# Kernel optimization log

Measured on AMD Instinct MI355X. Metric: run time of the kernel, lower is better.

The kernel has to match this reference:

```python
import jax, jax.numpy as jnp
import numpy as np

NUM_HEADS = 16
EPS = 1e-6  # torch LayerNorm default is 1e-5; module uses nn.LayerNorm default
LN_EPS = 1e-5


def layer_norm(x, w, b, eps=LN_EPS):
    # normalize over last dim (head_dim), matching infer_layer_norm
    mu = jnp.mean(x, axis=-1, keepdims=True)
    xc = x - mu
    var = jnp.mean(xc * xc, axis=-1, keepdims=True)
    return xc / jnp.sqrt(var + eps) * w + b


def setup_inputs() -> dict:
    key = jax.random.key(0)
    ks = jax.random.split(key, 4)
    B, N, C = 2, 4096, 1024
    H = NUM_HEADS
    D = C // H
    x = jax.random.normal(ks[0], (B, N, C), dtype=jnp.float32)
    qkv_w = jax.random.normal(ks[1], (3 * C, C), dtype=jnp.float32) * (C ** -0.5)
    qkv_b = jax.random.normal(ks[2], (3 * C,), dtype=jnp.float32) * 0.02
    q_norm_w = jnp.ones((D,), dtype=jnp.float32)
    q_norm_b = jnp.zeros((D,), dtype=jnp.float32)
    k_norm_w = jnp.ones((D,), dtype=jnp.float32)
    k_norm_b = jnp.zeros((D,), dtype=jnp.float32)
    proj_w = jax.random.normal(ks[3], (C, C), dtype=jnp.float32) * (C ** -0.5)
    proj_b = jnp.zeros((C,), dtype=jnp.float32)
    return {"x": x, "qkv_w": qkv_w, "qkv_b": qkv_b,
            "q_norm_w": q_norm_w, "q_norm_b": q_norm_b,
            "k_norm_w": k_norm_w, "k_norm_b": k_norm_b,
            "proj_w": proj_w, "proj_b": proj_b}


def reference(x, qkv_w, qkv_b, q_norm_w, q_norm_b, k_norm_w, k_norm_b, proj_w, proj_b):
    B, N, C = x.shape
    H = NUM_HEADS
    D = C // H
    scale = D ** -0.5
    # QKV projection: torch Linear uses y = x @ W^T + b
    qkv = x @ qkv_w.T + qkv_b                      # [B,N,3C]
    qkv = qkv.reshape(B, N, 3, H, D).transpose(2, 0, 3, 1, 4)  # [3,B,H,N,D]
    q, k, v = qkv[0], qkv[1], qkv[2]
    # per-head qk layernorm
    q = layer_norm(q, q_norm_w, q_norm_b)
    k = layer_norm(k, k_norm_w, k_norm_b)
    # scaled dot product attention
    attn = jnp.einsum('bhqd,bhkd->bhqk', q * scale, k)
    attn = jax.nn.softmax(attn, axis=-1)
    out = jnp.einsum('bhqk,bhkd->bhqd', attn, v)   # [B,H,N,D]
    out = out.transpose(0, 2, 1, 3).reshape(B, N, C)
    return out @ proj_w.T + proj_b
```

## Files before the change

### kernel.cpp

```cpp
#include <hip/hip_runtime.h>
#include <hip/hip_bf16.h>

#define NB 2
#define NN 4096
#define NC 1024
#define NH 16
#define ND 64
#define NM (NB*NN)
#define NK 1024
#define J_QKV 3072
#define QSCALE 0.18033688011112042f

typedef unsigned short u16;
typedef unsigned int   u32;
typedef __attribute__((ext_vector_type(8)))  __bf16 bf16x8;
typedef __attribute__((ext_vector_type(4)))  float  f32x4;
typedef __attribute__((ext_vector_type(16))) float  f32x16;

__device__ __forceinline__ u16 f2bf(float f) {
    unsigned int i = __builtin_bit_cast(unsigned int, f);
    unsigned int lsb = (i >> 16) & 1u;
    i += 0x7fffu + lsb;
    return (u16)(i >> 16);
}
__device__ __forceinline__ float fast_exp2(float x) {
#if __has_builtin(__builtin_amdgcn_exp2f)
    return __builtin_amdgcn_exp2f(x);
#else
    return exp2f(x);
#endif
}
__device__ __forceinline__ u32 pkbf(float a, float b) {
    u32 r;
    asm("v_cvt_pk_bf16_f32 %0, %1, %2" : "=v"(r) : "v"(a), "v"(b));
    return r;
}
typedef struct { u32 x, y; } u32pair;
__device__ __forceinline__ u32pair swap32(u32 a, u32 b) {
#if __has_builtin(__builtin_amdgcn_permlane32_swap)
    auto r = __builtin_amdgcn_permlane32_swap((int)a, (int)b, false, false);
    u32pair o; o.x = (u32)r[0]; o.y = (u32)r[1]; return o;
#else
    const bool hi = (threadIdx.x & 32) != 0;
    u32 as = (u32)__shfl_xor((int)a, 32);
    u32 bs = (u32)__shfl_xor((int)b, 32);
    u32pair o; o.x = hi ? bs : a; o.y = hi ? b : as; return o;
#endif
}

__device__ __forceinline__ void glds16(const u16* g, u16* l) {
    __builtin_amdgcn_global_load_lds(
        (const __attribute__((address_space(1))) u32*)g,
        (__attribute__((address_space(3))) u32*)l, 16, 0, 0);
}

__global__ __launch_bounds__(256) void cvt_bf16(
    const float* __restrict__ in, u16* __restrict__ out)
{
    const size_t i = ((size_t)blockIdx.x * 256 + threadIdx.x) * 8;
    const float4 a = *(const float4*)(in + i);
    const float4 b = *(const float4*)(in + i + 4);
    union { u16 h[8]; uint4 v; } u;
    u.h[0] = f2bf(a.x); u.h[1] = f2bf(a.y); u.h[2] = f2bf(a.z); u.h[3] = f2bf(a.w);
    u.h[4] = f2bf(b.x); u.h[5] = f2bf(b.y); u.h[6] = f2bf(b.z); u.h[7] = f2bf(b.w);
    *(uint4*)(out + i) = u.v;
}

template<int MODE, int NJB>
__global__ __launch_bounds__(256, 3) void gemm_nt(
    const u16* __restrict__ A, const u16* __restrict__ W,
    const float* __restrict__ bias,
    const float* __restrict__ qw, const float* __restrict__ qb,
    const float* __restrict__ kw, const float* __restrict__ kb,
    void* __restrict__ outv)
{
    __shared__ __align__(16) u16 AsL[128][32];
    __shared__ __align__(16) u16 AsH[128][32];
    __shared__ __align__(16) u16 BsL[128][32];
    __shared__ __align__(16) u16 BsH[128][32];
    const int t = threadIdx.x;
    const int w = t >> 6, lane = t & 63;
    const int nb   = blockIdx.x;
    const int cpx  = gridDim.x >> 3;
    const int nb2  = (nb & 7) * cpx + (nb >> 3);
    const int chunk = nb2 / cpx;
    const int c     = nb2 - chunk * cpx;
    const int jb  = (c >> 3) * 128;
    const int m0  = (chunk * 8 + (c & 7)) * 128;
    const int wr = (w >> 1) * 64, wc = (w & 1) * 64;
    const int srow = t >> 2, skc = (t & 3) * 8;
    const u16* ap0 = A + (size_t)(m0 + srow) * NK + skc;
    const u16* ap1 = ap0 + (size_t)64 * NK;
    const u16* wp0 = W + (size_t)(jb + srow) * NK + skc;
    const u16* wp1 = wp0 + (size_t)64 * NK;
    u16* asl0 = &AsL[srow][skc];    u16* asl1 = &AsL[srow + 64][skc];
    u16* ash0 = &AsH[srow][skc];    u16* ash1 = &AsH[srow + 64][skc];
    u16* bsl0 = &BsL[srow][skc];    u16* bsl1 = &BsL[srow + 64][skc];
    u16* bsh0 = &BsH[srow][skc];    u16* bsh1 = &BsH[srow + 64][skc];
    const int fm = lane & 15, fk = 8 * (lane >> 4);
    f32x4 acc[4][4];
    #pragma unroll
    for (int i = 0; i < 4; ++i)
        #pragma unroll
        for (int j = 0; j < 4; ++j) acc[i][j] = (f32x4){0.f, 0.f, 0.f, 0.f};

    for (int kt = 0; kt < NK / 64; ++kt) {
        const int ko = kt * 64;
        glds16(ap0 + ko, asl0);
        glds16(ap1 + ko, asl1);
        glds16(ap0 + ko + 32, ash0);
        glds16(ap1 + ko + 32, ash1);
        glds16(wp0 + ko, bsl0);
        glds16(wp1 + ko, bsl1);
        glds16(wp0 + ko + 32, bsh0);
        glds16(wp1 + ko + 32, bsh1);
        __syncthreads();
        {
            bf16x8 af[4], bfr[4];
            #pragma unroll
            for (int i = 0; i < 4; ++i) af[i]  = *(const bf16x8*)&AsL[wr + 16 * i + fm][fk];
            #pragma unroll
            for (int j = 0; j < 4; ++j) bfr[j] = *(const bf16x8*)&BsL[wc + 16 * j + fm][fk];
            #pragma unroll
            for (int i = 0; i < 4; ++i)
                #pragma unroll
                for (int j = 0; j < 4; ++j)
                    acc[i][j] = __builtin_amdgcn_mfma_f32_16x16x32_bf16(af[i], bfr[j], acc[i][j], 0, 0, 0);
        }
        {
            bf16x8 af[4], bfr[4];
            #pragma unroll
            for (int i = 0; i < 4; ++i) af[i]  = *(const bf16x8*)&AsH[wr + 16 * i + fm][fk];
            #pragma unroll
            for (int j = 0; j < 4; ++j) bfr[j] = *(const bf16x8*)&BsH[wc + 16 * j + fm][fk];
            #pragma unroll
            for (int i = 0; i < 4; ++i)
                #pragma unroll
                for (int j = 0; j < 4; ++j)
                    acc[i][j] = __builtin_amdgcn_mfma_f32_16x16x32_bf16(af[i], bfr[j], acc[i][j], 0, 0, 0);
        }
        __syncthreads();
    }
    const int c16 = lane & 15;
    float bv[4];
    #pragma unroll
    for (int j = 0; j < 4; ++j) bv[j] = bias[jb + wc + 16 * j + c16];
    #pragma unroll
    for (int i = 0; i < 4; ++i)
        #pragma unroll
        for (int j = 0; j < 4; ++j)
            #pragma unroll
            for (int r = 0; r < 4; ++r) acc[i][j][r] += bv[j];
    if (MODE == 0) {
        const int s = jb >> 10;
        if (s < 2) {
            const float* lw = s ? kw : qw;
            const float* lb = s ? kb : qb;
            float lwv[4], lbv[4];
            #pragma unroll
            for (int j = 0; j < 4; ++j) {
                lwv[j] = lw[16 * j + c16]; lbv[j] = lb[16 * j + c16];
            }
            #pragma unroll
            for (int i = 0; i < 4; ++i)
                #pragma unroll
                for (int r = 0; r < 4; ++r) {
                    float sum = acc[i][0][r] + acc[i][1][r] + acc[i][2][r] + acc[i][3][r];
                    #pragma unroll
                    for (int off = 1; off < 16; off <<= 1) sum += __shfl_xor(sum, off);
                    const float mu = sum * (1.0f / 64.0f);
                    float v2 = 0.f;
                    #pragma unroll
                    for (int j = 0; j < 4; ++j) { const float dd = acc[i][j][r] - mu; v2 += dd * dd; }
                    #pragma unroll
                    for (int off = 1; off < 16; off <<= 1) v2 += __shfl_xor(v2, off);
                    const float rstd = rsqrtf(v2 * (1.0f / 64.0f) + 1e-5f);
                    #pragma unroll
                    for (int j = 0; j < 4; ++j) {
                        float y = (acc[i][j][r] - mu) * rstd * lwv[j] + lbv[j];
                        if (s == 0) y *= QSCALE;
                        acc[i][j][r] = y;
                    }
                }
        }
        u16* out = (u16*)outv;
        const int r0 = 4 * (lane >> 4);
        #pragma unroll
        for (int j = 0; j < 4; ++j) {
            const int col = jb + wc + 16 * j + c16;
            const int ss = col >> 10, hh = (col >> 6) & 15, d = col & 63;
            #pragma unroll
            for (int i = 0; i < 4; ++i)
                #pragma unroll
                for (int r = 0; r < 4; ++r) {
                    const int row = m0 + wr + 16 * i + r0 + r;
                    const int b = row >> 12, n = row & 4095;
                    out[((((size_t)ss * NB + b) * NH + hh) * NN + n) * ND + d] = f2bf(acc[i][j][r]);
                }
        }
    } else {
        float* out = (float*)outv;
        const int r0 = 4 * (lane >> 4);
        #pragma unroll
        for (int i = 0; i < 4; ++i)
            #pragma unroll
            for (int r = 0; r < 4; ++r) {
                const int row = m0 + wr + 16 * i + r0 + r;
                #pragma unroll
                for (int j = 0; j < 4; ++j)
                    out[(size_t)row * NC + jb + wc + 16 * j + c16] = acc[i][j][r];
            }
    }
}

__global__ __launch_bounds__(256, 2) void attn_mfma(
    const u16* __restrict__ qkv, u16* __restrict__ aout)
{
    __shared__ __align__(16) u16 Ks[2][64][72];
    __shared__ __align__(16) u16 Vt[2][64][72];
    const int bid  = blockIdx.x;
    const int qblk = bid & 15;
    const int bh   = bid >> 4;
    const int b = bh >> 4, hh = bh & 15;
    const size_t plane = (size_t)NB * NH * NN * ND;
    const size_t base  = ((size_t)(b * NH + hh)) * NN * ND;
    const u16* qp = qkv + base;
    const u16* kp = qkv + plane + base;
    const u16* vp = qkv + 2 * plane + base;
    const int t = threadIdx.x, w = t >> 6, lane = t & 63;
    const int half = lane >> 5, m32 = lane & 31;
    const int q0 = qblk * 256 + 64 * w;

    bf16x8 qf[2][4];
    #pragma unroll
    for (int s = 0; s < 2; ++s) {
        const u16* qrow = qp + (size_t)(q0 + 32 * s + m32) * ND + 8 * half;
        #pragma unroll
        for (int kt = 0; kt < 4; ++kt) qf[s][kt] = *(const bf16x8*)(qrow + 16 * kt);
    }
    f32x16 O[2][2], z;
    #pragma unroll
    for (int r = 0; r < 16; ++r) { O[0][0][r] = 0.f; O[0][1][r] = 0.f;
                                   O[1][0][r] = 0.f; O[1][1][r] = 0.f; z[r] = 0.f; }
    float lpart[2] = {0.f, 0.f};

    const int dgK = 16 * w;
    const int kp2 = t & 31, dgV = (t >> 5) * 8;
    const u16* ksrc = kp + (size_t)lane * ND + dgK;
    const u16* vsrc = vp + (size_t)(2 * kp2) * ND + dgV;

    uint4 kr0, kr1, vre, vro;
    kr0 = *(const uint4*)(ksrc);
    kr1 = *(const uint4*)(ksrc + 8);
    vre = *(const uint4*)(vsrc);
    vro = *(const uint4*)(vsrc + ND);
    {
        *(uint4*)&Ks[0][lane][dgK]     = kr0;
        *(uint4*)&Ks[0][lane][dgK + 8] = kr1;
        const u32* ew = (const u32*)&vre;
        const u32* ow = (const u32*)&vro;
        #pragma unroll
        for (int d = 0; d < 4; ++d) {
            u32 lo = __builtin_amdgcn_perm(ow[d], ew[d], 0x05040100u);
            u32 hi = __builtin_amdgcn_perm(ow[d], ew[d], 0x07060302u);
            *(u32*)&Vt[0][dgV + 2 * d][2 * kp2]     = lo;
            *(u32*)&Vt[0][dgV + 2 * d + 1][2 * kp2] = hi;
        }
    }
    __syncthreads();

    union W8 { u32 wd[4]; bf16x8 f; };

    for (int kb = 0; kb < NN / 64; ++kb) {
        const int cur = kb & 1, nxt = cur ^ 1;
        const bool more = (kb + 1) < (NN / 64);
        if (more) {
            const u16* ks2 = ksrc + (size_t)(kb + 1) * 64 * ND;
            kr0 = *(const uint4*)ks2;
            kr1 = *(const uint4*)(ks2 + 8);
            const u16* vs2 = vsrc + (size_t)(kb + 1) * 64 * ND;
            vre = *(const uint4*)vs2;
            vro = *(const uint4*)(vs2 + ND);
        }
        f32x16 sT0[2], sT1[2];
        __builtin_amdgcn_s_setprio(1);
        {
            bf16x8 k0 = *(const bf16x8*)&Ks[cur][m32][8 * half];
            bf16x8 k1 = *(const bf16x8*)&Ks[cur][32 + m32][8 * half];
            sT0[0] = __builtin_amdgcn_mfma_f32_32x32x16_bf16(k0, qf[0][0], z, 0, 0, 0);
            sT0[1] = __builtin_amdgcn_mfma_f32_32x32x16_bf16(k1, qf[0][0], z, 0, 0, 0);
        }
        #pragma unroll
        for (int kt = 1; kt < 4; ++kt) {
            bf16x8 k0 = *(const bf16x8*)&Ks[cur][m32][16 * kt + 8 * half];
            bf16x8 k1 = *(const bf16x8*)&Ks[cur][32 + m32][16 * kt + 8 * half];
            sT0[0] = __builtin_amdgcn_mfma_f32_32x32x16_bf16(k0, qf[0][kt], sT0[0], 0, 0, 0);
            sT0[1] = __builtin_amdgcn_mfma_f32_32x32x16_bf16(k1, qf[0][kt], sT0[1], 0, 0, 0);
        }
        {
            bf16x8 k0 = *(const bf16x8*)&Ks[cur][m32][8 * half];
            bf16x8 k1 = *(const bf16x8*)&Ks[cur][32 + m32][8 * half];
            sT1[0] = __builtin_amdgcn_mfma_f32_32x32x16_bf16(k0, qf[1][0], z, 0, 0, 0);
            sT1[1] = __builtin_amdgcn_mfma_f32_32x32x16_bf16(k1, qf[1][0], z, 0, 0, 0);
        }
        #pragma unroll
        for (int kt = 1; kt < 4; ++kt) {
            bf16x8 k0 = *(const bf16x8*)&Ks[cur][m32][16 * kt + 8 * half];
            bf16x8 k1 = *(const bf16x8*)&Ks[cur][32 + m32][16 * kt + 8 * half];
            sT1[0] = __builtin_amdgcn_mfma_f32_32x32x16_bf16(k0, qf[1][kt], sT1[0], 0, 0, 0);
            sT1[1] = __builtin_amdgcn_mfma_f32_32x32x16_bf16(k1, qf[1][kt], sT1[1], 0, 0, 0);
        }
        __builtin_amdgcn_s_setprio(0);
        W8 pa0[4], pa1[4];
        {
            float ss0 = 0.f, ss1 = 0.f;
            #pragma unroll
            for (int kh = 0; kh < 2; ++kh) {
                float p[16];
                #pragma unroll
                for (int r = 0; r < 16; ++r) p[r] = fast_exp2(sT0[kh][r]);
                #pragma unroll
                for (int r = 0; r < 8; ++r) { ss0 += p[r]; ss1 += p[8 + r]; }
                u32 c[4][2];
                #pragma unroll
                for (int g = 0; g < 4; ++g) {
                    c[g][0] = pkbf(p[4 * g + 0], p[4 * g + 1]);
                    c[g][1] = pkbf(p[4 * g + 2], p[4 * g + 3]);
                }
                #pragma unroll
                for (int par = 0; par < 2; ++par) {
                    u32pair wA = swap32(c[2 * par][0], c[2 * par + 1][0]);
                    u32pair wB = swap32(c[2 * par][1], c[2 * par + 1][1]);
                    const int kt = 2 * kh + par;
                    pa0[kt].wd[0] = wA.x;
                    pa0[kt].wd[1] = wB.x;
                    pa0[kt].wd[2] = wA.y;
                    pa0[kt].wd[3] = wB.y;
                }
            }
            lpart[0] += ss0 + ss1;
        }
        __builtin_amdgcn_s_setprio(1);
        #pragma unroll
        for (int kt = 0; kt < 4; ++kt) {
            bf16x8 v0 = *(const bf16x8*)&Vt[cur][m32][16 * kt + 8 * half];
            bf16x8 v1 = *(const bf16x8*)&Vt[cur][32 + m32][16 * kt + 8 * half];
            O[0][0] = __builtin_amdgcn_mfma_f32_32x32x16_bf16(pa0[kt].f, v0, O[0][0], 0, 0, 0);
            O[0][1] = __builtin_amdgcn_mfma_f32_32x32x16_bf16(pa0[kt].f, v1, O[0][1], 0, 0, 0);
        }
        __builtin_amdgcn_s_setprio(0);
        {
            float ss0 = 0.f, ss1 = 0.f;
            #pragma unroll
            for (int kh = 0; kh < 2; ++kh) {
                float p[16];
                #pragma unroll
                for (int r = 0; r < 16; ++r) p[r] = fast_exp2(sT1[kh][r]);
                #pragma unroll
                for (int r = 0; r < 8; ++r) { ss0 += p[r]; ss1 += p[8 + r]; }
                u32 c[4][2];
                #pragma unroll
                for (int g = 0; g < 4; ++g) {
                    c[g][0] = pkbf(p[4 * g + 0], p[4 * g + 1]);
                    c[g][1] = pkbf(p[4 * g + 2], p[4 * g + 3]);
                }
                #pragma unroll
                for (int par = 0; par < 2; ++par) {
                    u32pair wA = swap32(c[2 * par][0], c[2 * par + 1][0]);
                    u32pair wB = swap32(c[2 * par][1], c[2 * par + 1][1]);
                    const int kt = 2 * kh + par;
                    pa1[kt].wd[0] = wA.x;
                    pa1[kt].wd[1] = wB.x;
                    pa1[kt].wd[2] = wA.y;
                    pa1[kt].wd[3] = wB.y;
                }
            }
            lpart[1] += ss0 + ss1;
        }
        __builtin_amdgcn_s_setprio(1);
        #pragma unroll
        for (int kt = 0; kt < 4; ++kt) {
            bf16x8 v0 = *(const bf16x8*)&Vt[cur][m32][16 * kt + 8 * half];
            bf16x8 v1 = *(const bf16x8*)&Vt[cur][32 + m32][16 * kt + 8 * half];
            O[1][0] = __builtin_amdgcn_mfma_f32_32x32x16_bf16(pa1[kt].f, v0, O[1][0], 0, 0, 0);
            O[1][1] = __builtin_amdgcn_mfma_f32_32x32x16_bf16(pa1[kt].f, v1, O[1][1], 0, 0, 0);
        }
        __builtin_amdgcn_s_setprio(0);
        if (more) {
            *(uint4*)&Ks[nxt][lane][dgK]     = kr0;
            *(uint4*)&Ks[nxt][lane][dgK + 8] = kr1;
            const u32* ew = (const u32*)&vre;
            const u32* ow = (const u32*)&vro;
            #pragma unroll
            for (int d = 0; d < 4; ++d) {
                u32 lo = __builtin_amdgcn_perm(ow[d], ew[d], 0x05040100u);
                u32 hi = __builtin_amdgcn_perm(ow[d], ew[d], 0x07060302u);
                *(u32*)&Vt[nxt][dgV + 2 * d][2 * kp2]     = lo;
                *(u32*)&Vt[nxt][dgV + 2 * d + 1][2 * kp2] = hi;
            }
            __syncthreads();
        }
    }
    #pragma unroll
    for (int s = 0; s < 2; ++s) {
        const float tot = lpart[s] + __shfl_xor(lpart[s], 32);
        #pragma unroll
        for (int r = 0; r < 16; ++r) {
            const int qq = (r & 3) + 8 * (r >> 2) + 4 * half;
            const float inv = 1.0f / __shfl(tot, qq);
            const int row = q0 + 32 * s + qq;
            u16* dst = aout + ((size_t)(b * NN + row)) * NC + hh * 64;
            dst[m32]      = f2bf(O[s][0][r] * inv);
            dst[32 + m32] = f2bf(O[s][1][r] * inv);
        }
    }
}

extern "C" void kernel_launch(void* const* d_in, const int* in_sizes, int n_in,
                              void* d_out, int out_size, void* d_ws, size_t ws_size,
                              hipStream_t stream) {
    const float* x     = (const float*)d_in[0];
    const float* qkv_w = (const float*)d_in[1];
    const float* qkv_b = (const float*)d_in[2];
    const float* q_nw  = (const float*)d_in[3];
    const float* q_nb  = (const float*)d_in[4];
    const float* k_nw  = (const float*)d_in[5];
    const float* k_nb  = (const float*)d_in[6];
    const float* p_w   = (const float*)d_in[7];
    const float* p_b   = (const float*)d_in[8];
    float* out = (float*)d_out;
    u16* qkv    = (u16*)d_ws;
    u16* x_bf   = qkv + (size_t)3 * NB * NH * NN * ND;
    u16* attn_o = x_bf;
    u16* w_bf   = x_bf + (size_t)NM * NC;
    u16* pw_bf  = w_bf + (size_t)J_QKV * NK;

    cvt_bf16<<<(NM * NC) / 2048, 256, 0, stream>>>(x, x_bf);
    cvt_bf16<<<(J_QKV * NK) / 2048, 256, 0, stream>>>(qkv_w, w_bf);
    cvt_bf16<<<(NC * NK) / 2048, 256, 0, stream>>>(p_w, pw_bf);

    gemm_nt<0, J_QKV / 128><<<(J_QKV / 128) * (NM / 128), 256, 0, stream>>>(
        x_bf, w_bf, qkv_b, q_nw, q_nb, k_nw, k_nb, qkv);
    attn_mfma<<<NB * NH * (NN / 256), 256, 0, stream>>>(qkv, attn_o);
    gemm_nt<1, NC / 128><<<(NC / 128) * (NM / 128), 256, 0, stream>>>(
        attn_o, pw_bf, p_b, q_nw, q_nb, k_nw, k_nb, out);
}
```

Measured before the change: 332.4 us.

## Double-buffer GEMM shared-memory tiles with async global-to-LDS prefetch

Turns the GEMM main loop into a two-stage pipeline. The A/B shared tiles are doubled, and the tile for iteration kt+2 is issued with global_load_lds while the current tile feeds the MFMAs, with explicit vmcnt waits and barriers replacing __syncthreads. The goal is to hide global memory latency behind compute. In exchange, LDS use doubles and the occupancy hint drops from 3 to 2 blocks per CU.

New measurement: 341.9 us. 1.03x slower.

```diff
diff --git a/kernel.cpp b/kernel.cpp
--- a/kernel.cpp
+++ b/kernel.cpp
@@ -67,17 +67,15 @@
 }
 
 template<int MODE, int NJB>
-__global__ __launch_bounds__(256, 3) void gemm_nt(
+__global__ __launch_bounds__(256, 2) void gemm_nt(
     const u16* __restrict__ A, const u16* __restrict__ W,
     const float* __restrict__ bias,
     const float* __restrict__ qw, const float* __restrict__ qb,
     const float* __restrict__ kw, const float* __restrict__ kb,
     void* __restrict__ outv)
 {
-    __shared__ __align__(16) u16 AsL[128][32];
-    __shared__ __align__(16) u16 AsH[128][32];
-    __shared__ __align__(16) u16 BsL[128][32];
-    __shared__ __align__(16) u16 BsH[128][32];
+    __shared__ __align__(16) u16 As[2][2][128][32];
+    __shared__ __align__(16) u16 Bs[2][2][128][32];
     const int t = threadIdx.x;
     const int w = t >> 6, lane = t & 63;
     const int nb   = blockIdx.x;
@@ -93,10 +91,6 @@
     const u16* ap1 = ap0 + (size_t)64 * NK;
     const u16* wp0 = W + (size_t)(jb + srow) * NK + skc;
     const u16* wp1 = wp0 + (size_t)64 * NK;
-    u16* asl0 = &AsL[srow][skc];    u16* asl1 = &AsL[srow + 64][skc];
-    u16* ash0 = &AsH[srow][skc];    u16* ash1 = &AsH[srow + 64][skc];
-    u16* bsl0 = &BsL[srow][skc];    u16* bsl1 = &BsL[srow + 64][skc];
-    u16* bsh0 = &BsH[srow][skc];    u16* bsh1 = &BsH[srow + 64][skc];
     const int fm = lane & 15, fk = 8 * (lane >> 4);
     f32x4 acc[4][4];
     #pragma unroll
@@ -104,43 +98,50 @@
         #pragma unroll
         for (int j = 0; j < 4; ++j) acc[i][j] = (f32x4){0.f, 0.f, 0.f, 0.f};
 
+#define STAGE(ktile, d) do {                                      \
+        const int ko_ = (ktile) * 64;                             \
+        glds16(ap0 + ko_,      &As[d][0][srow][skc]);             \
+        glds16(ap1 + ko_,      &As[d][0][srow + 64][skc]);        \
+        glds16(ap0 + ko_ + 32, &As[d][1][srow][skc]);             \
+        glds16(ap1 + ko_ + 32, &As[d][1][srow + 64][skc]);        \
+        glds16(wp0 + ko_,      &Bs[d][0][srow][skc]);             \
+        glds16(wp1 + ko_,      &Bs[d][0][srow + 64][skc]);        \
+        glds16(wp0 + ko_ + 32, &Bs[d][1][srow][skc]);             \
+        glds16(wp1 + ko_ + 32, &Bs[d][1][srow + 64][skc]);        \
+    } while (0)
+
+    STAGE(0, 0);
+    STAGE(1, 1);
+    asm volatile("s_waitcnt vmcnt(8)" ::: "memory");
+    asm volatile("s_barrier" ::: "memory");
+
     for (int kt = 0; kt < NK / 64; ++kt) {
-        const int ko = kt * 64;
-        glds16(ap0 + ko, asl0);
-        glds16(ap1 + ko, asl1);
-        glds16(ap0 + ko + 32, ash0);
-        glds16(ap1 + ko + 32, ash1);
-        glds16(wp0 + ko, bsl0);
-        glds16(wp1 + ko, bsl1);
-        glds16(wp0 + ko + 32, bsh0);
-        glds16(wp1 + ko + 32, bsh1);
-        __syncthreads();
-        {
+        const int cur = kt & 1;
+        #pragma unroll
+        for (int h = 0; h < 2; ++h) {
             bf16x8 af[4], bfr[4];
             #pragma unroll
-            for (int i = 0; i < 4; ++i) af[i]  = *(const bf16x8*)&AsL[wr + 16 * i + fm][fk];
-            #pragma unroll
-            for (int j = 0; j < 4; ++j) bfr[j] = *(const bf16x8*)&BsL[wc + 16 * j + fm][fk];
+            for (int i = 0; i < 4; ++i) af[i]  = *(const bf16x8*)&As[cur][h][wr + 16 * i + fm][fk];
+            #pragma unroll
+            for (int j = 0; j < 4; ++j) bfr[j] = *(const bf16x8*)&Bs[cur][h][wc + 16 * j + fm][fk];
             #pragma unroll
             for (int i = 0; i < 4; ++i)
                 #pragma unroll
                 for (int j = 0; j < 4; ++j)
                     acc[i][j] = __builtin_amdgcn_mfma_f32_16x16x32_bf16(af[i], bfr[j], acc[i][j], 0, 0, 0);
         }
-        {
-            bf16x8 af[4], bfr[4];
-            #pragma unroll
-            for (int i = 0; i < 4; ++i) af[i]  = *(const bf16x8*)&AsH[wr + 16 * i + fm][fk];
-            #pragma unroll
-            for (int j = 0; j < 4; ++j) bfr[j] = *(const bf16x8*)&BsH[wc + 16 * j + fm][fk];
-            #pragma unroll
-            for (int i = 0; i < 4; ++i)
-                #pragma unroll
-                for (int j = 0; j < 4; ++j)
-                    acc[i][j] = __builtin_amdgcn_mfma_f32_16x16x32_bf16(af[i], bfr[j], acc[i][j], 0, 0, 0);
-        }
-        __syncthreads();
-    }
+        asm volatile("s_waitcnt lgkmcnt(0)" ::: "memory");
+        asm volatile("s_barrier" ::: "memory");
+        if (kt + 2 < NK / 64) {
+            STAGE(kt + 2, cur);
+            asm volatile("s_waitcnt vmcnt(8)" ::: "memory");
+        } else {
+            asm volatile("s_waitcnt vmcnt(0)" ::: "memory");
+        }
+        asm volatile("s_barrier" ::: "memory");
+    }
+#undef STAGE
+
     const int c16 = lane & 15;
     float bv[4];
     #pragma unroll
```
